# Kernel optimization log

Hardware: AMD Instinct MI355X
Metric: run time of the kernel (lower is better)

## Reference

```python
import jax, jax.numpy as jnp
import numpy as np

N_POINTS = 32768
K = 16
N_EDGES = N_POINTS * K
IN_CH, OUT_CH = 3, 1
HID, LIFT, PROJ = 64, 256, 256
N_LAYERS = 4
POS_DIM = 2


def _lin_init(key, fan_in, fan_out):
    return jax.random.normal(key, (fan_in, fan_out), jnp.float32) / np.sqrt(fan_in)


def setup_inputs() -> dict:
    key = jax.random.key(0)
    ks = jax.random.split(key, 16)
    x = jax.random.normal(ks[0], (2, N_POINTS, IN_CH), jnp.float32)
    pos = jax.random.uniform(ks[1], (N_POINTS, POS_DIM), jnp.float32)
    edge_index = jax.random.randint(ks[2], (2, N_EDGES), 0, N_POINTS, jnp.int64)
    eff_in = IN_CH + POS_DIM
    kin = HID + 2 * POS_DIM  # concat(pos_src, pos_dst, x_src)
    return {
        "x": x,
        "pos": pos,
        "edge_index": edge_index,
        "lift_w1": _lin_init(ks[3], eff_in, LIFT),
        "lift_b1": jnp.zeros((LIFT,), jnp.float32),
        "lift_w2": _lin_init(ks[4], LIFT, HID),
        "lift_b2": jnp.zeros((HID,), jnp.float32),
        "kW1": jax.random.normal(ks[5], (N_LAYERS, kin, HID), jnp.float32) / np.sqrt(kin),
        "kb1": jnp.zeros((N_LAYERS, HID), jnp.float32),
        "kW2": jax.random.normal(ks[6], (N_LAYERS, HID, HID), jnp.float32) / np.sqrt(HID),
        "kb2": jnp.zeros((N_LAYERS, HID), jnp.float32),
        "proj_w1": _lin_init(ks[7], HID, PROJ),
        "proj_b1": jnp.zeros((PROJ,), jnp.float32),
        "proj_w2": _lin_init(ks[8], PROJ, OUT_CH),
        "proj_b2": jnp.zeros((OUT_CH,), jnp.float32),
    }


def _gelu(v):
    return jax.nn.gelu(v, approximate=False)  # torch nn.GELU default (exact)


def reference(x, pos, edge_index, lift_w1, lift_b1, lift_w2, lift_b2,
              kW1, kb1, kW2, kb2, proj_w1, proj_b1, proj_w2, proj_b2):
    B, n, _ = x.shape
    posb = jnp.broadcast_to(pos[None], (B, n, pos.shape[-1]))
    # lift: Linear -> GELU -> Linear on concat([x, pos])
    h = jnp.concatenate([x, posb], axis=-1)
    h = _gelu(h @ lift_w1 + lift_b1) @ lift_w2 + lift_b2  # [B, n, HID]

    src, dst = edge_index[0], edge_index[1]
    pos_e = jnp.concatenate([pos[src], pos[dst]], axis=-1)  # [E, 2*POS_DIM]
    cnt = jax.ops.segment_sum(jnp.ones((src.shape[0],), h.dtype), dst, num_segments=n)
    cnt = jnp.maximum(cnt, 1.0)[None, :, None]

    for l in range(kW1.shape[0]):
        xj = h[:, src]  # gather neighbor features [B, E, HID]
        e = jnp.concatenate([jnp.broadcast_to(pos_e[None], (B,) + pos_e.shape), xj], axis=-1)
        m = _gelu(e @ kW1[l] + kb1[l]) @ kW2[l] + kb2[l]  # edge messages [B, E, HID]
        agg = jax.vmap(lambda mb: jax.ops.segment_sum(mb, dst, num_segments=n))(m)
        h = h + agg / cnt  # mean aggregation + residual skip

    out = _gelu(h @ proj_w1 + proj_b1) @ proj_w2 + proj_b2  # [B, n, OUT_CH]
    return out.transpose(0, 2, 1)  # [B, OUT_CH, n]
```

## Files before the change

### kernel.cpp

```cpp
#include <hip/hip_runtime.h>
#include <cstdint>
#include <cstddef>

#define N_POINTS 32768
#define KDEG 16
#define N_EDGES (N_POINTS*KDEG)
#define BATCH 2
#define HID 64
#define LIFTD 256
#define PROJD 256
#define KIN 68
#define NLAYERS 4

#define DSTS 32
#define LK_WAVES 4
#define GSTR 72
#define MSTR 65

#define LASTR 40
#define LGSTR 264

#define FR_EDGE 0
#define FR_LW1  80
#define FR_LW2  96
#define FR_TOT  128

typedef unsigned short ushort_t;
typedef short short8 __attribute__((ext_vector_type(8)));
typedef float floatx4 __attribute__((ext_vector_type(4)));

union frag_u { uint4 u; short8 s; };

__device__ __forceinline__ float gelu_f(float x) {
    return 0.5f * x * (1.0f + erff(x * 0.70710678118654752440f));
}
__device__ __forceinline__ float gelu_fast(float x) {
    float t = x * x;
    float inner = x * fmaf(0.044715f, t, 1.0f);
    float e = __expf(-1.5957691216f * inner);
    return x * __frcp_rn(1.0f + e);
}

__device__ __forceinline__ ushort_t f2bf(float x) {
    unsigned int u = __float_as_uint(x);
    unsigned int r = (u + 0x7FFFu + ((u >> 16) & 1u)) >> 16;
    return (ushort_t)r;
}
__device__ __forceinline__ unsigned int pk2bf(float a, float b) {
    return (unsigned int)f2bf(a) | ((unsigned int)f2bf(b) << 16);
}

__global__ void hist_kernel(const int* __restrict__ ei, int* __restrict__ counts) {
    int e = blockIdx.x * 256 + threadIdx.x;
    if (e < N_EDGES) atomicAdd(&counts[ei[N_EDGES + e]], 1);
}

__global__ void scan_kernel(const int* __restrict__ counts, int* __restrict__ row_start) {
    __shared__ int sums[1024];
    const int tid = threadIdx.x;
    const int base = tid * 32;
    int s = 0;
    for (int i = 0; i < 32; ++i) s += counts[base + i];
    sums[tid] = s;
    __syncthreads();
    const int own = s;
    for (int off = 1; off < 1024; off <<= 1) {
        int v = (tid >= off) ? sums[tid - off] : 0;
        __syncthreads();
        sums[tid] += v;
        __syncthreads();
    }
    int run = sums[tid] - own;
    for (int i = 0; i < 32; ++i) { row_start[base + i] = run; run += counts[base + i]; }
    if (tid == 1023) row_start[N_POINTS] = N_EDGES;
}

__global__ void fill_kernel(const int* __restrict__ ei, const int* __restrict__ row_start,
                            int* __restrict__ cursor, int2* __restrict__ csr_pair) {
    int e = blockIdx.x * 256 + threadIdx.x;
    if (e < N_EDGES) {
        int s = ei[e], d = ei[N_EDGES + e];
        int p = atomicAdd(&cursor[d], 1);
        csr_pair[row_start[d] + p] = make_int2(s, d);
    }
}

__global__ void wprep_kernel(const float* __restrict__ kW1, const float* __restrict__ kb1,
                             const float* __restrict__ kW2,
                             const float* __restrict__ lw1, const float* __restrict__ lb1,
                             const float* __restrict__ lw2,
                             ushort_t* __restrict__ wfrag) {
    int t = blockIdx.x * 256 + threadIdx.x;
    if (t >= FR_TOT * 64) return;
    const int lane = t & 63;
    const int fi = t >> 6;
    const int m16 = lane & 15;
    const int qb = ((lane >> 4) & 3) * 8;
    ushort_t o[8];
    if (fi < FR_LW1) {
        const int l = fi / 20, f = fi % 20;
        const int n = ((f < 12 ? (f & 3) : ((f - 12) & 3)) * 16) + m16;
        if (f < 12) {
            const int kc = f >> 2;
            const float* W1 = kW1 + (size_t)l * KIN * HID;
            const float* B1 = kb1 + (size_t)l * HID;
#pragma unroll
            for (int j = 0; j < 8; ++j) {
                const int k = kc * 32 + qb + j;
                float v;
                if (k < 64) v = W1[(size_t)(4 + k) * HID + n];
                else if (k < 68) v = W1[(size_t)(k - 64) * HID + n];
                else if (k == 68) v = B1[n];
                else v = 0.f;
                o[j] = f2bf(v);
            }
        } else {
            const int kc = (f - 12) >> 2;
            const float* W2 = kW2 + (size_t)l * HID * HID;
#pragma unroll
            for (int j = 0; j < 8; ++j)
                o[j] = f2bf(W2[(size_t)(kc * 32 + qb + j) * HID + n]);
        }
    } else if (fi < FR_LW2) {
        const int ct = fi - FR_LW1;
        const int n = ct * 16 + m16;
#pragma unroll
        for (int j = 0; j < 8; ++j) {
            const int k = qb + j;
            float v;
            if (k < 5) v = lw1[(size_t)k * LIFTD + n];
            else if (k == 5) v = lb1[n];
            else v = 0.f;
            o[j] = f2bf(v);
        }
    } else {
        const int idx = fi - FR_LW2;
        const int kc = idx >> 2, ct = idx & 3;
        const int n = ct * 16 + m16;
#pragma unroll
        for (int j = 0; j < 8; ++j)
            o[j] = f2bf(lw2[(size_t)(kc * 32 + qb + j) * HID + n]);
    }
    ushort_t* dst = wfrag + ((size_t)fi * 64 + lane) * 8;
#pragma unroll
    for (int j = 0; j < 8; ++j) dst[j] = o[j];
}

__global__ void wprep_proj_kernel(const float* __restrict__ pw1, ushort_t* __restrict__ pfrag) {
    int t = blockIdx.x * 256 + threadIdx.x;
    if (t >= 32 * 64) return;
    const int lane = t & 63;
    const int fi = t >> 6;
    const int kc = fi >> 4, ct = fi & 15;
    const int n = ct * 16 + (lane & 15);
    const int qb = ((lane >> 4) & 3) * 8;
    ushort_t* dst = pfrag + ((size_t)fi * 64 + lane) * 8;
#pragma unroll
    for (int j = 0; j < 8; ++j)
        dst[j] = f2bf(pw1[(size_t)(kc * 32 + qb + j) * PROJD + n]);
}

__global__ __launch_bounds__(256) void lift_kernel(
    const float* __restrict__ x, const float* __restrict__ pos,
    const ushort_t* __restrict__ wfrag, const float* __restrict__ lb2,
    float* __restrict__ hres, ushort_t* __restrict__ hb16)
{
    __shared__ __align__(16) ushort_t WF[3072 * 8];
    __shared__ __align__(16) ushort_t LA[4][16 * LASTR];
    __shared__ __align__(16) ushort_t LG[4][16 * LGSTR];

    const int tid = threadIdx.x;
    const int wv = tid >> 6;
    const int lane = tid & 63;
    const int m16 = lane & 15;
    const int q = lane >> 4;

    {
        const uint4* gw = (const uint4*)(wfrag + (size_t)FR_LW1 * 64 * 8);
        uint4* lw = (uint4*)WF;
        for (int i = tid; i < 3072; i += 256) lw[i] = gw[i];
    }
    __syncthreads();

    ushort_t* At = &LA[wv][0];
    ushort_t* Gt = &LG[wv][0];

    float b2r[4];
#pragma unroll
    for (int ct = 0; ct < 4; ++ct) b2r[ct] = lb2[ct * 16 + m16];

    for (int grp = 0; grp < 4; ++grp) {
        const int gid0 = (blockIdx.x * 16 + wv * 4 + grp) * 16;

        if (lane < 16) {
            const int g = gid0 + lane;
            const int i = g & (N_POINTS - 1);
            const float x0 = x[3 * (size_t)g], x1 = x[3 * (size_t)g + 1], x2 = x[3 * (size_t)g + 2];
            const float2 p = *(const float2*)(pos + 2 * i);
            uint4 w;
            w.x = pk2bf(x0, x1);
            w.y = pk2bf(x2, p.x);
            w.z = pk2bf(p.y, 1.0f);
            w.w = 0u;
            uint4 z; z.x = z.y = z.z = z.w = 0u;
            *(uint4*)&At[lane * LASTR + 0] = w;
            *(uint4*)&At[lane * LASTR + 8] = z;
            *(uint4*)&At[lane * LASTR + 16] = z;
            *(uint4*)&At[lane * LASTR + 24] = z;
        }

        const short8 a = *(const short8*)&At[m16 * LASTR + q * 8];
        floatx4 acc[16];
#pragma unroll
        for (int ct = 0; ct < 16; ++ct) {
            const short8 bf = *(const short8*)&WF[((size_t)ct * 64 + lane) * 8];
            floatx4 c = {0.f, 0.f, 0.f, 0.f};
            acc[ct] = __builtin_amdgcn_mfma_f32_16x16x32_bf16(a, bf, c, 0, 0, 0);
        }

#pragma unroll
        for (int ct = 0; ct < 16; ++ct)
#pragma unroll
            for (int r = 0; r < 4; ++r)
                Gt[(q * 4 + r) * LGSTR + ct * 16 + m16] = f2bf(gelu_fast(acc[ct][r]));

        floatx4 acc2[4];
#pragma unroll
        for (int ct = 0; ct < 4; ++ct) { floatx4 z = {0.f, 0.f, 0.f, 0.f}; acc2[ct] = z; }
#pragma unroll
        for (int kc = 0; kc < 8; ++kc) {
            const short8 g = *(const short8*)&Gt[m16 * LGSTR + kc * 32 + q * 8];
#pragma unroll
            for (int ct = 0; ct < 4; ++ct) {
                const short8 bf = *(const short8*)&WF[((size_t)(1024 + (kc * 4 + ct) * 64) + lane) * 8];
                acc2[ct] = __builtin_amdgcn_mfma_f32_16x16x32_bf16(g, bf, acc2[ct], 0, 0, 0);
            }
        }

#pragma unroll
        for (int ct = 0; ct < 4; ++ct)
#pragma unroll
            for (int r = 0; r < 4; ++r) {
                const float v = acc2[ct][r] + b2r[ct];
                const size_t idx = (size_t)(gid0 + q * 4 + r) * HID + ct * 16 + m16;
                hres[idx] = v;
                hb16[idx] = f2bf(v);
            }
    }
}

__global__ __launch_bounds__(256, 4) void layer_kernel(
    float* __restrict__ hres,
    const ushort_t* __restrict__ hb_in,
    ushort_t* __restrict__ hb_out,
    const float* __restrict__ pos,
    const int2* __restrict__ csr_pair,
    const int* __restrict__ row_start, const int* __restrict__ counts,
    const ushort_t* __restrict__ wfrag, const float* __restrict__ B2)
{
    __shared__ __align__(16) float GMt[LK_WAVES][16 * MSTR];
    __shared__ float hacc[DSTS * HID];
    __shared__ int   segb[LK_WAVES][16];

    const int b = blockIdx.y;
    const int dstBase = blockIdx.x * DSTS;
    const int tid = threadIdx.x;
    const int wv = tid >> 6;
    const int lane = tid & 63;
    const int m16 = lane & 15;
    const int q = lane >> 4;
    const int ch = lane & 3;
    const int growL = lane >> 2;
    const int permSrc = m16 * 4 + q;

    for (int i = tid; i < DSTS * HID; i += 256) hacc[i] = 0.f;

    const short8* wf = (const short8*)wfrag;
    short8 w1f[3][4], w2f[2][4];
#pragma unroll
    for (int kc = 0; kc < 3; ++kc)
#pragma unroll
        for (int ct = 0; ct < 4; ++ct) w1f[kc][ct] = wf[(kc * 4 + ct) * 64 + lane];
#pragma unroll
    for (int kc = 0; kc < 2; ++kc)
#pragma unroll
        for (int ct = 0; ct < 4; ++ct) w2f[kc][ct] = wf[(12 + kc * 4 + ct) * 64 + lane];
    float b2r[4];
#pragma unroll
    for (int ct = 0; ct < 4; ++ct) b2r[ct] = B2[ct * 16 + m16];
    __syncthreads();

    const int estart = row_start[dstBase];
    const int eend   = row_start[dstBase + DSTS];
    const int ntiles = (eend - estart + 15) >> 4;
    const int elast  = (eend > 0) ? (eend - 1) : 0;
    const ushort_t* __restrict__ hb = hb_in + (size_t)b * N_POINTS * HID;

    float* GM = &GMt[wv][0];
    ushort_t* Gt = (ushort_t*)GM;

    frag_u hC0, hC1; uint4 pwC; int segC;
    {
        const int e0 = estart + wv * 16;
        const int2 pA = csr_pair[min(e0 + growL, elast)];
        const int2 pB = csr_pair[min(e0 + m16, elast)];
        const uint4* hr = (const uint4*)(hb + (size_t)pA.x * HID);
        hC0.u = hr[ch];
        hC1.u = hr[ch + 4];
        const float2 ps = *(const float2*)(pos + 2 * pB.x);
        const float2 pd = *(const float2*)(pos + 2 * pB.y);
        pwC.x = pk2bf(ps.x, ps.y);
        pwC.y = pk2bf(pd.x, pd.y);
        pwC.z = 0x00003F80u;
        pwC.w = 0u;
        segC = (e0 + m16 < eend) ? (pB.y - dstBase) : -1;
    }

    for (int t = wv; t < ntiles; t += LK_WAVES) {
        frag_u hN0, hN1; uint4 pwN; int segN;
        {
            const int e0n = estart + (t + LK_WAVES) * 16;
            const int2 pA = csr_pair[min(e0n + growL, elast)];
            const int2 pB = csr_pair[min(e0n + m16, elast)];
            const uint4* hr = (const uint4*)(hb + (size_t)pA.x * HID);
            hN0.u = hr[ch];
            hN1.u = hr[ch + 4];
            const float2 ps = *(const float2*)(pos + 2 * pB.x);
            const float2 pd = *(const float2*)(pos + 2 * pB.y);
            pwN.x = pk2bf(ps.x, ps.y);
            pwN.y = pk2bf(pd.x, pd.y);
            pwN.z = 0x00003F80u;
            pwN.w = 0u;
            segN = (e0n + m16 < eend) ? (pB.y - dstBase) : -1;
        }

        if (lane < 16) segb[wv][lane] = segC;

        frag_u a0, a1, a2;
        a0.u.x = (unsigned)__shfl((int)hC0.u.x, permSrc);
        a0.u.y = (unsigned)__shfl((int)hC0.u.y, permSrc);
        a0.u.z = (unsigned)__shfl((int)hC0.u.z, permSrc);
        a0.u.w = (unsigned)__shfl((int)hC0.u.w, permSrc);
        a1.u.x = (unsigned)__shfl((int)hC1.u.x, permSrc);
        a1.u.y = (unsigned)__shfl((int)hC1.u.y, permSrc);
        a1.u.z = (unsigned)__shfl((int)hC1.u.z, permSrc);
        a1.u.w = (unsigned)__shfl((int)hC1.u.w, permSrc);
        if (q == 0) { a2.u = pwC; }
        else        { a2.u.x = 0u; a2.u.y = 0u; a2.u.z = 0u; a2.u.w = 0u; }

        floatx4 acc[4];
#pragma unroll
        for (int ct = 0; ct < 4; ++ct) {
            floatx4 c = {0.f, 0.f, 0.f, 0.f};
            c = __builtin_amdgcn_mfma_f32_16x16x32_bf16(a0.s, w1f[0][ct], c, 0, 0, 0);
            c = __builtin_amdgcn_mfma_f32_16x16x32_bf16(a1.s, w1f[1][ct], c, 0, 0, 0);
            c = __builtin_amdgcn_mfma_f32_16x16x32_bf16(a2.s, w1f[2][ct], c, 0, 0, 0);
            acc[ct] = c;
        }

#pragma unroll
        for (int ct = 0; ct < 4; ++ct)
#pragma unroll
            for (int r = 0; r < 4; ++r)
                Gt[(q * 4 + r) * GSTR + ct * 16 + m16] = f2bf(gelu_fast(acc[ct][r]));

        short8 g0 = *(const short8*)&Gt[m16 * GSTR +  0 + q * 8];
        short8 g1 = *(const short8*)&Gt[m16 * GSTR + 32 + q * 8];
        floatx4 mm[4];
#pragma unroll
        for (int ct = 0; ct < 4; ++ct) {
            floatx4 c = {0.f, 0.f, 0.f, 0.f};
            c = __builtin_amdgcn_mfma_f32_16x16x32_bf16(g0, w2f[0][ct], c, 0, 0, 0);
            c = __builtin_amdgcn_mfma_f32_16x16x32_bf16(g1, w2f[1][ct], c, 0, 0, 0);
            mm[ct] = c;
        }

#pragma unroll
        for (int ct = 0; ct < 4; ++ct)
#pragma unroll
            for (int r = 0; r < 4; ++r)
                GM[(q * 4 + r) * MSTR + ct * 16 + m16] = mm[ct][r] + b2r[ct];

        {
            float racc = 0.f;
            int rseg = -1;
#pragma unroll
            for (int r = 0; r < 16; ++r) {
                const int s = segb[wv][r];
                const float v = GM[r * MSTR + lane];
                if (s != rseg) {
                    if (rseg >= 0) atomicAdd(&hacc[rseg * HID + lane], racc);
                    rseg = s;
                    racc = v;
                } else {
                    racc += v;
                }
            }
            if (rseg >= 0) atomicAdd(&hacc[rseg * HID + lane], racc);
        }

        hC0 = hN0; hC1 = hN1; pwC = pwN; segC = segN;
    }
    __syncthreads();

    const size_t rowbase = (size_t)b * N_POINTS * HID;
    for (int i = tid; i < DSTS * HID; i += 256) {
        const int dl = i >> 6, c = i & 63;
        const int node = dstBase + dl;
        const float cnt = fmaxf((float)counts[node], 1.f);
        const size_t off = rowbase + (size_t)node * HID + c;
        const float v = hres[off] + hacc[i] / cnt;
        hres[off] = v;
        hb_out[off] = f2bf(v);
    }
}

__global__ __launch_bounds__(256) void proj_kernel(
    const ushort_t* __restrict__ hbm, const ushort_t* __restrict__ pfrag,
    const float* __restrict__ b1, const float* __restrict__ w2,
    const float* __restrict__ b2, float* __restrict__ out)
{
    __shared__ __align__(16) ushort_t WF[2048 * 8];

    const int tid = threadIdx.x;
    const int wv = tid >> 6;
    const int lane = tid & 63;
    const int m16 = lane & 15;
    const int q = lane >> 4;

    {
        const uint4* gw = (const uint4*)pfrag;
        uint4* lw = (uint4*)WF;
        for (int i = tid; i < 2048; i += 256) lw[i] = gw[i];
    }
    __syncthreads();

    float b1v[16], w2v[16];
#pragma unroll
    for (int ct = 0; ct < 16; ++ct) {
        b1v[ct] = b1[ct * 16 + m16];
        w2v[ct] = w2[ct * 16 + m16];
    }
    const float b2s = b2[0];

    for (int grp = 0; grp < 4; ++grp) {
        const int gid0 = (blockIdx.x * 16 + wv * 4 + grp) * 16;

        frag_u a0, a1;
        const uint4* hr = (const uint4*)(hbm + (size_t)(gid0 + m16) * HID);
        a0.u = hr[q];
        a1.u = hr[4 + q];

        floatx4 acc[16];
#pragma unroll
        for (int ct = 0; ct < 16; ++ct) {
            const short8 bf0 = *(const short8*)&WF[((size_t)(ct) * 64 + lane) * 8];
            const short8 bf1 = *(const short8*)&WF[((size_t)(16 + ct) * 64 + lane) * 8];
            floatx4 c = {0.f, 0.f, 0.f, 0.f};
            c = __builtin_amdgcn_mfma_f32_16x16x32_bf16(a0.s, bf0, c, 0, 0, 0);
            c = __builtin_amdgcn_mfma_f32_16x16x32_bf16(a1.s, bf1, c, 0, 0, 0);
            acc[ct] = c;
        }

        float p[4] = {0.f, 0.f, 0.f, 0.f};
#pragma unroll
        for (int ct = 0; ct < 16; ++ct)
#pragma unroll
            for (int r = 0; r < 4; ++r)
                p[r] += gelu_f(acc[ct][r] + b1v[ct]) * w2v[ct];

#pragma unroll
        for (int r = 0; r < 4; ++r) {
            p[r] += __shfl_xor(p[r], 1);
            p[r] += __shfl_xor(p[r], 2);
            p[r] += __shfl_xor(p[r], 4);
            p[r] += __shfl_xor(p[r], 8);
        }
        if (m16 == 0) {
#pragma unroll
            for (int r = 0; r < 4; ++r)
                out[gid0 + q * 4 + r] = p[r] + b2s;
        }
    }
}

extern "C" void kernel_launch(void* const* d_in, const int* in_sizes, int n_in,
                              void* d_out, int out_size, void* d_ws, size_t ws_size,
                              hipStream_t stream)
{
    const float* x        = (const float*)d_in[0];
    const float* pos      = (const float*)d_in[1];
    const int*   ei       = (const int*)d_in[2];
    const float* lift_w1  = (const float*)d_in[3];
    const float* lift_b1  = (const float*)d_in[4];
    const float* lift_w2  = (const float*)d_in[5];
    const float* lift_b2  = (const float*)d_in[6];
    const float* kW1      = (const float*)d_in[7];
    const float* kb1      = (const float*)d_in[8];
    const float* kW2      = (const float*)d_in[9];
    const float* kb2      = (const float*)d_in[10];
    const float* proj_w1  = (const float*)d_in[11];
    const float* proj_b1  = (const float*)d_in[12];
    const float* proj_w2  = (const float*)d_in[13];
    const float* proj_b2  = (const float*)d_in[14];
    float* out = (float*)d_out;

    char* ws = (char*)d_ws;
    size_t off = 0;
    float*    hres  = (float*)(ws + off);    off += (size_t)BATCH * N_POINTS * HID * 4;
    ushort_t* hbA   = (ushort_t*)(ws + off); off += (size_t)BATCH * N_POINTS * HID * 2;
    ushort_t* hbB   = (ushort_t*)(ws + off); off += (size_t)BATCH * N_POINTS * HID * 2;
    int* counts     = (int*)(ws + off);      off += (size_t)N_POINTS * 4;
    int* row_start  = (int*)(ws + off);      off += (size_t)(N_POINTS + 4) * 4;
    int* cursor     = (int*)(ws + off);      off += (size_t)N_POINTS * 4;
    int2* csr_pair  = (int2*)(ws + off);     off += (size_t)N_EDGES * 8;
    ushort_t* wfrag = (ushort_t*)cursor;
    ushort_t* pfrag = (ushort_t*)csr_pair;

    hipMemsetAsync(counts, 0, N_POINTS * 4, stream);
    hipMemsetAsync(cursor, 0, N_POINTS * 4, stream);

    hist_kernel<<<N_EDGES / 256, 256, 0, stream>>>(ei, counts);
    scan_kernel<<<1, 1024, 0, stream>>>(counts, row_start);
    fill_kernel<<<N_EDGES / 256, 256, 0, stream>>>(ei, row_start, cursor, csr_pair);
    wprep_kernel<<<(FR_TOT * 64) / 256, 256, 0, stream>>>(
        kW1, kb1, kW2, lift_w1, lift_b1, lift_w2, wfrag);

    lift_kernel<<<BATCH * N_POINTS / 256, 256, 0, stream>>>(x, pos, wfrag, lift_b2, hres, hbA);

    ushort_t* hin = hbA;
    ushort_t* hout = hbB;
    for (int l = 0; l < NLAYERS; ++l) {
        layer_kernel<<<dim3(N_POINTS / DSTS, BATCH), 256, 0, stream>>>(
            hres, hin, hout, pos, csr_pair, row_start, counts,
            wfrag + (size_t)l * 20 * 64 * 8, kb2 + (size_t)l * HID);
        ushort_t* tmp = hin; hin = hout; hout = tmp;
    }

    wprep_proj_kernel<<<(32 * 64) / 256, 256, 0, stream>>>(proj_w1, pfrag);
    proj_kernel<<<BATCH * N_POINTS / 256, 256, 0, stream>>>(
        hin, pfrag, proj_b1, proj_w2, proj_b2, out);
}
```

Measured before the change: 655.1 us.

## Accumulate edge messages directly from MFMA registers into duplicated shared accumulators

Instead of staging the 16x64 message tile in a per-wave shared buffer and reducing it row by row, each lane now run-length reduces its four MFMA output rows in registers and atomically adds into one of two padded shared accumulator copies, chosen by quadrant, which cuts the shared round-trip and the contention on each address. The second-layer weights move from registers into shared memory to lower register pressure. The bias is folded into the final mean by adding B2 once for nodes with edges. This trades extra shared reads of the weights for fewer stores and less LDS traffic.

```diff
diff --git a/kernel.cpp b/kernel.cpp
--- a/kernel.cpp
+++ b/kernel.cpp
@@ -15,7 +15,8 @@
 #define DSTS 32
 #define LK_WAVES 4
 #define GSTR 72
-#define MSTR 65
+#define HSTR2 65
+#define HCPY (DSTS * HSTR2)
 
 #define LASTR 40
 #define LGSTR 264
@@ -258,9 +259,9 @@
     const int* __restrict__ row_start, const int* __restrict__ counts,
     const ushort_t* __restrict__ wfrag, const float* __restrict__ B2)
 {
-    __shared__ __align__(16) float GMt[LK_WAVES][16 * MSTR];
-    __shared__ float hacc[DSTS * HID];
-    __shared__ int   segb[LK_WAVES][16];
+    __shared__ __align__(16) ushort_t Gts[LK_WAVES][16 * GSTR];
+    __shared__ float hacc[2 * HCPY];
+    __shared__ __align__(16) uint4 WL2[8 * 64];
 
     const int b = blockIdx.y;
     const int dstBase = blockIdx.x * DSTS;
@@ -273,21 +274,19 @@
     const int growL = lane >> 2;
     const int permSrc = m16 * 4 + q;
 
-    for (int i = tid; i < DSTS * HID; i += 256) hacc[i] = 0.f;
+    for (int i = tid; i < 2 * HCPY; i += 256) hacc[i] = 0.f;
+
+    {
+        const uint4* gw = (const uint4*)(wfrag + (size_t)12 * 64 * 8);
+        for (int i = tid; i < 8 * 64; i += 256) WL2[i] = gw[i];
+    }
 
     const short8* wf = (const short8*)wfrag;
-    short8 w1f[3][4], w2f[2][4];
+    short8 w1f[3][4];
 #pragma unroll
     for (int kc = 0; kc < 3; ++kc)
 #pragma unroll
         for (int ct = 0; ct < 4; ++ct) w1f[kc][ct] = wf[(kc * 4 + ct) * 64 + lane];
-#pragma unroll
-    for (int kc = 0; kc < 2; ++kc)
-#pragma unroll
-        for (int ct = 0; ct < 4; ++ct) w2f[kc][ct] = wf[(12 + kc * 4 + ct) * 64 + lane];
-    float b2r[4];
-#pragma unroll
-    for (int ct = 0; ct < 4; ++ct) b2r[ct] = B2[ct * 16 + m16];
     __syncthreads();
 
     const int estart = row_start[dstBase];
@@ -296,8 +295,8 @@
     const int elast  = (eend > 0) ? (eend - 1) : 0;
     const ushort_t* __restrict__ hb = hb_in + (size_t)b * N_POINTS * HID;
 
-    float* GM = &GMt[wv][0];
-    ushort_t* Gt = (ushort_t*)GM;
+    ushort_t* Gt = &Gts[wv][0];
+    float* hcp = &hacc[(q & 1) * HCPY];
 
     frag_u hC0, hC1; uint4 pwC; int segC;
     {
@@ -334,7 +333,9 @@
             segN = (e0n + m16 < eend) ? (pB.y - dstBase) : -1;
         }
 
-        if (lane < 16) segb[wv][lane] = segC;
+        int ss[4];
+#pragma unroll
+        for (int r = 0; r < 4; ++r) ss[r] = __shfl(segC, q * 4 + r);
 
         frag_u a0, a1, a2;
         a0.u.x = (unsigned)__shfl((int)hC0.u.x, permSrc);
@@ -369,34 +370,31 @@
         floatx4 mm[4];
 #pragma unroll
         for (int ct = 0; ct < 4; ++ct) {
+            frag_u wa0, wa1;
+            wa0.u = WL2[(0 * 4 + ct) * 64 + lane];
+            wa1.u = WL2[(1 * 4 + ct) * 64 + lane];
             floatx4 c = {0.f, 0.f, 0.f, 0.f};
-            c = __builtin_amdgcn_mfma_f32_16x16x32_bf16(g0, w2f[0][ct], c, 0, 0, 0);
-            c = __builtin_amdgcn_mfma_f32_16x16x32_bf16(g1, w2f[1][ct], c, 0, 0, 0);
+            c = __builtin_amdgcn_mfma_f32_16x16x32_bf16(g0, wa0.s, c, 0, 0, 0);
+            c = __builtin_amdgcn_mfma_f32_16x16x32_bf16(g1, wa1.s, c, 0, 0, 0);
             mm[ct] = c;
         }
 
 #pragma unroll
-        for (int ct = 0; ct < 4; ++ct)
-#pragma unroll
-            for (int r = 0; r < 4; ++r)
-                GM[(q * 4 + r) * MSTR + ct * 16 + m16] = mm[ct][r] + b2r[ct];
-
-        {
-            float racc = 0.f;
-            int rseg = -1;
-#pragma unroll
-            for (int r = 0; r < 16; ++r) {
-                const int s = segb[wv][r];
-                const float v = GM[r * MSTR + lane];
-                if (s != rseg) {
-                    if (rseg >= 0) atomicAdd(&hacc[rseg * HID + lane], racc);
-                    rseg = s;
-                    racc = v;
+        for (int ct = 0; ct < 4; ++ct) {
+            const int colb = ct * 16 + m16;
+            float run = mm[ct][0];
+            int cs = ss[0];
+#pragma unroll
+            for (int r = 1; r < 4; ++r) {
+                if (ss[r] == cs) {
+                    run += mm[ct][r];
                 } else {
-                    racc += v;
+                    if (cs >= 0) atomicAdd(&hcp[cs * HSTR2 + colb], run);
+                    cs = ss[r];
+                    run = mm[ct][r];
                 }
             }
-            if (rseg >= 0) atomicAdd(&hacc[rseg * HID + lane], racc);
+            if (cs >= 0) atomicAdd(&hcp[cs * HSTR2 + colb], run);
         }
 
         hC0 = hN0; hC1 = hN1; pwC = pwN; segC = segN;
@@ -407,9 +405,11 @@
     for (int i = tid; i < DSTS * HID; i += 256) {
         const int dl = i >> 6, c = i & 63;
         const int node = dstBase + dl;
-        const float cnt = fmaxf((float)counts[node], 1.f);
+        const int cntv = counts[node];
+        const float cl = fmaxf((float)cntv, 1.f);
+        const float s = hacc[dl * HSTR2 + c] + hacc[HCPY + dl * HSTR2 + c];
         const size_t off = rowbase + (size_t)node * HID + c;
-        const float v = hres[off] + hacc[i] / cnt;
+        const float v = hres[off] + s / cl + (cntv > 0 ? B2[c] : 0.f);
         hres[off] = v;
         hb_out[off] = f2bf(v);
     }
```

New measurement: 752.4 us. 1.15x slower.
